# Kernel tuning notes

Measured on AMD Instinct MI355X. Metric: run time of the kernel, lower is better.

## Reference

```python
import jax, jax.numpy as jnp
import numpy as np

B, T, V, H = 256, 2048, 128, 64  # batch, seq_len, vocab/input_size, hidden_size


def setup_inputs() -> dict:
    key = jax.random.key(0)
    ks = jax.random.split(key, 11)
    s = 0.1  # weight scale
    d = jnp.float32
    return {
        "x": jax.random.normal(ks[0], (B, T, V), dtype=d),
        "W_f": jax.random.normal(ks[1], (V + H, H), dtype=d) * s,
        "b_f": jax.random.normal(ks[2], (H,), dtype=d) * s,
        "W_if": jax.random.normal(ks[3], (V + H, H), dtype=d) * s,
        "b_if": jax.random.normal(ks[4], (H,), dtype=d) * s,
        "W_ic": jax.random.normal(ks[5], (V + H, H), dtype=d) * s,
        "b_ic": jax.random.normal(ks[6], (H,), dtype=d) * s,
        "W_o": jax.random.normal(ks[7], (V + H, H), dtype=d) * s,
        "b_o": jax.random.normal(ks[8], (H,), dtype=d) * s,
        "W_out": jax.random.normal(ks[9], (H, V), dtype=d) * s,
        "b_out": jax.random.normal(ks[10], (V,), dtype=d) * s,
    }


def reference(x, W_f, b_f, W_if, b_if, W_ic, b_ic, W_o, b_o, W_out, b_out):
    # Manual LSTM cell from the source, stepped over time with lax.scan.
    # Per step (faithful to forward()+getOut()):
    #   s = concat(x_t, h);  f = sigmoid(s@W_f+b_f);  c = c*f
    #   add = tanh(s@W_ic+b_ic); af = sigmoid(s@W_if+b_if); c = c + add*af
    #   o = sigmoid(s@W_o+b_o);  h = tanh(c)*o
    #   out = softmax(h@W_out+b_out)
    b, t = x.shape[0], x.shape[1]
    h0 = jnp.zeros((b, W_f.shape[1]), dtype=x.dtype)
    c0 = jnp.zeros_like(h0)

    def step(carry, x_t):
        h, c = carry
        s = jnp.concatenate([x_t, h], axis=1)          # [B, V+H]
        f = jax.nn.sigmoid(s @ W_f + b_f)
        add = jnp.tanh(s @ W_ic + b_ic)
        af = jax.nn.sigmoid(s @ W_if + b_if)
        c = c * f + add * af
        o = jax.nn.sigmoid(s @ W_o + b_o)
        h = jnp.tanh(c) * o
        out = jax.nn.softmax(h @ W_out + b_out, axis=-1)  # [B, V]
        return (h, c), out

    (_, _), outs = jax.lax.scan(step, (h0, c0), jnp.swapaxes(x, 0, 1))
    return jnp.swapaxes(outs, 0, 1)  # [B, T, V]
```

## Files before the change

kernel.cpp:

```cpp
#include <hip/hip_runtime.h>
#include <cstdint>
#include <cstddef>

#define BB 256
#define TT 2048
#define VV 128
#define HH 64

typedef __attribute__((ext_vector_type(8))) short short8;
typedef __attribute__((ext_vector_type(4))) float f32x4;
typedef __attribute__((ext_vector_type(2))) float f32x2;

__device__ __forceinline__ float frcp(float x){ return __builtin_amdgcn_rcpf(x); }
__device__ __forceinline__ float sigm(float x){ return frcp(1.f + __expf(-x)); }
__device__ __forceinline__ float tanh_f(float x){ return 1.f - 2.f*frcp(1.f + __expf(2.f*x)); }

__device__ __forceinline__ void bar_lds(){
  asm volatile("s_waitcnt lgkmcnt(0)" ::: "memory");
  __builtin_amdgcn_s_barrier();
  __builtin_amdgcn_sched_barrier(0);
}

__device__ __forceinline__ void gload16(const void* g, void* l){
  __builtin_amdgcn_global_load_lds(
      (const __attribute__((address_space(1))) void*)g,
      (__attribute__((address_space(3))) void*)l, 16, 0, 0);
}

__device__ __forceinline__ unsigned short bf16hi(float x){
  unsigned u = __float_as_uint(x);
  return (unsigned short)((u + 0x7fffu + ((u>>16)&1u)) >> 16);
}
__device__ __forceinline__ void splitpack(const float* v8, short8& hi, short8& lo){
  #pragma unroll
  for (int j=0;j<8;++j){
    unsigned short h = bf16hi(v8[j]);
    float fh = __uint_as_float(((unsigned)h)<<16);
    unsigned short lw = bf16hi(v8[j] - fh);
    hi[j] = (short)h; lo[j] = (short)lw;
  }
}

__device__ __forceinline__ float qsum(float v){
  int t1 = __builtin_amdgcn_update_dpp(0, __float_as_int(v), 0xB1, 0xF, 0xF, true);
  v += __int_as_float(t1);
  int t2 = __builtin_amdgcn_update_dpp(0, __float_as_int(v), 0x4E, 0xF, 0xF, true);
  v += __int_as_float(t2);
  return v;
}

template<int CTRL>
__device__ __forceinline__ float dppmov(float v){
  return __int_as_float(__builtin_amdgcn_update_dpp(0, __float_as_int(v), CTRL, 0xF, 0xF, true));
}

__device__ __forceinline__ void pkfma(f32x2& acc, f32x2 a, f32x2 b){
  asm volatile("v_pk_fma_f32 %0, %1, %2, %0" : "+v"(acc) : "v"(a), "v"(b));
}

__global__ __launch_bounds__(256) void conv_w_k(
  const float* __restrict__ Wf, const float* __restrict__ Wi,
  const float* __restrict__ Wc, const float* __restrict__ Wo,
  const float* __restrict__ Wout,
  unsigned short* __restrict__ W4h, unsigned short* __restrict__ W4l,
  unsigned short* __restrict__ WOh, unsigned short* __restrict__ WOl)
{
  const int idx = blockIdx.x*256 + threadIdx.x;
  if (idx < 32768){
    const int j = idx&7, l=(idx>>3)&63, kk=(idx>>9)&3, nt=idx>>11;
    const int k = kk*32 + (l>>4)*8 + j;
    const int n = nt*16 + (l&15);
    const int g = n&3, colw = n>>2;
    const float* Ws = (g==0)?Wf:((g==1)?Wi:((g==2)?Wc:Wo));
    const float v = Ws[k*HH + colw];
    const unsigned short h = bf16hi(v);
    const float fh = __uint_as_float(((unsigned)h)<<16);
    W4h[idx] = h; W4l[idx] = bf16hi(v - fh);
  }
  if (idx < 8192){
    const int j = idx&7, l=(idx>>3)&63, kk=(idx>>9)&1, jt=idx>>10;
    const int k = kk*32 + (l>>4)*8 + j;
    const int jc = jt*16 + (l&15);
    const float v = Wout[k*VV + jc];
    const unsigned short h = bf16hi(v);
    const float fh = __uint_as_float(((unsigned)h)<<16);
    WOh[idx] = h; WOl[idx] = bf16hi(v - fh);
  }
}

__global__ __launch_bounds__(512,1) void pre_gemm_k(
  const float* __restrict__ x, const unsigned short* __restrict__ W4h,
  const unsigned short* __restrict__ W4l, float* __restrict__ PRE)
{
  __shared__ __align__(16) unsigned short XFh[16384];
  __shared__ __align__(16) unsigned short XFl[16384];
  const int tid = threadIdx.x, wv = tid>>6, l = tid&63, b = blockIdx.x;

  short8 Bh[2][4], Bl[2][4];
  #pragma unroll
  for (int ntl=0; ntl<2; ++ntl){
    const int nt = wv*2 + ntl;
    #pragma unroll
    for (int kk=0; kk<4; ++kk){
      Bh[ntl][kk] = *(const short8*)(W4h + ((nt*4+kk)*64 + l)*8);
      Bl[ntl][kk] = *(const short8*)(W4l + ((nt*4+kk)*64 + l)*8);
    }
  }

  #pragma unroll 1
  for (int mt=0; mt<16; ++mt){
    const size_t base_row = (size_t)b*TT + mt*128;
    #pragma unroll
    for (int i=0;i<4;++i){
      const int G = tid*4+i;
      const int lf = G&63, kk=(G>>6)&3, m8=G>>8;
      const float* src = x + (base_row + m8*16 + (lf&15))*VV + kk*32 + (lf>>4)*8;
      const f32x4 u = *(const f32x4*)src;
      const f32x4 v = *(const f32x4*)(src+4);
      float tmp[8] = {u[0],u[1],u[2],u[3], v[0],v[1],v[2],v[3]};
      short8 hi, lo; splitpack(tmp, hi, lo);
      *(short8*)&XFh[(size_t)G*8] = hi;
      *(short8*)&XFl[(size_t)G*8] = lo;
    }
    bar_lds();
    for (int m8=0; m8<8; ++m8){
      short8 Ah[4], Al[4];
      #pragma unroll
      for (int kk=0;kk<4;++kk){
        Ah[kk] = *(const short8*)&XFh[((m8*4+kk)*64 + l)*8];
        Al[kk] = *(const short8*)&XFl[((m8*4+kk)*64 + l)*8];
      }
      #pragma unroll
      for (int ntl=0; ntl<2; ++ntl){
        f32x4 acc = {0.f,0.f,0.f,0.f};
        #pragma unroll
        for (int kk=0;kk<4;++kk){
          acc = __builtin_amdgcn_mfma_f32_16x16x32_bf16(Al[kk], Bh[ntl][kk], acc, 0,0,0);
          acc = __builtin_amdgcn_mfma_f32_16x16x32_bf16(Ah[kk], Bl[ntl][kk], acc, 0,0,0);
          acc = __builtin_amdgcn_mfma_f32_16x16x32_bf16(Ah[kk], Bh[ntl][kk], acc, 0,0,0);
        }
        const int nt = wv*2 + ntl;
        float* dst = PRE + (base_row + m8*16 + (l>>4)*4)*256 + nt*16 + (l&15);
        #pragma unroll
        for (int r=0;r<4;++r) dst[(size_t)r*256] = acc[r];
      }
    }
    bar_lds();
  }
}

__global__ __launch_bounds__(256,1) void recur8_k(
  const float* __restrict__ W_f, const float* __restrict__ b_f,
  const float* __restrict__ W_if, const float* __restrict__ b_if,
  const float* __restrict__ W_ic, const float* __restrict__ b_ic,
  const float* __restrict__ W_o,  const float* __restrict__ b_o,
  const float* __restrict__ PRE,  float* __restrict__ H)
{
  __shared__ __align__(16) float hring[32*HH];
  const int tid=threadIdx.x, wv=tid>>6, l=tid&63, b=blockIdx.x;
  const int col = wv*16 + (l>>2), q = l&3;
  const bool qb0 = (l&1)!=0, qb1 = (l&2)!=0;

  f32x2 wf2[8], wi2[8], wc2[8], wo2[8];
  #pragma unroll
  for (int m=0;m<8;++m){
    const size_t k0 = (size_t)(VV + q*16 + 2*m)*HH + col;
    wf2[m] = f32x2{W_f [k0], W_f [k0+HH]};
    wi2[m] = f32x2{W_if[k0], W_if[k0+HH]};
    wc2[m] = f32x2{W_ic[k0], W_ic[k0+HH]};
    wo2[m] = f32x2{W_o [k0], W_o [k0+HH]};
  }
  const float bq  = ((q==0)?b_f:(q==1)?b_if:(q==2)?b_ic:b_o)[col];
  const float sgn = (q==2)? 2.f : -1.f;
  const float aA  = (q==2)? -2.f : 1.f;
  const float aB  = (q==2)? 1.f : 0.f;

  const float* PREl = PRE + (size_t)b*TT*256 + wv*64 + l;
  float* Hb = H + (size_t)b*TT*HH;
  const f32x4* hring4 = (const f32x4*)hring;

  if (tid < HH) hring[31*HH + tid] = 0.f;

  float pf[8];
  #pragma unroll
  for (int j=0;j<8;++j) pf[j] = PREl[(size_t)j*256];

  bar_lds();

  float c_ = 0.f;
  int hoff = 31*16 + q*4;
  int woff = col;

  #pragma unroll 1
  for (int t8=0; t8<TT; t8+=8){
    #pragma unroll
    for (int j=0;j<8;++j){
      const int t = t8+j;
      if (wv==1 && t>0 && (t&15)==0){
        #pragma unroll
        for (int i=0;i<4;++i){
          const int rt = t-16 + i*4 + (l>>4);
          const f32x4 v = hring4[(rt&31)*16 + (l&15)];
          *(f32x4*)(Hb + (size_t)rt*HH + (l&15)*4) = v;
        }
      }
      const f32x4 h0 = hring4[hoff+0], h1 = hring4[hoff+1];
      const f32x4 h2 = hring4[hoff+2], h3 = hring4[hoff+3];
      const float nxt = PREl[(size_t)((t+8)&(TT-1))*256];
      const float pq = pf[j];
      f32x2 a0={0.f,0.f}, a1={0.f,0.f}, a2={0.f,0.f}, a3={0.f,0.f};
      {
        const f32x2 p0 = f32x2{h0[0],h0[1]}, p1 = f32x2{h0[2],h0[3]};
        const f32x2 p2 = f32x2{h1[0],h1[1]}, p3 = f32x2{h1[2],h1[3]};
        const f32x2 p4 = f32x2{h2[0],h2[1]}, p5 = f32x2{h2[2],h2[3]};
        const f32x2 p6 = f32x2{h3[0],h3[1]}, p7 = f32x2{h3[2],h3[3]};
        pkfma(a0,p0,wf2[0]); pkfma(a0,p1,wf2[1]); pkfma(a0,p2,wf2[2]); pkfma(a0,p3,wf2[3]);
        pkfma(a0,p4,wf2[4]); pkfma(a0,p5,wf2[5]); pkfma(a0,p6,wf2[6]); pkfma(a0,p7,wf2[7]);
        pkfma(a1,p0,wi2[0]); pkfma(a1,p1,wi2[1]); pkfma(a1,p2,wi2[2]); pkfma(a1,p3,wi2[3]);
        pkfma(a1,p4,wi2[4]); pkfma(a1,p5,wi2[5]); pkfma(a1,p6,wi2[6]); pkfma(a1,p7,wi2[7]);
        pkfma(a2,p0,wc2[0]); pkfma(a2,p1,wc2[1]); pkfma(a2,p2,wc2[2]); pkfma(a2,p3,wc2[3]);
        pkfma(a2,p4,wc2[4]); pkfma(a2,p5,wc2[5]); pkfma(a2,p6,wc2[6]); pkfma(a2,p7,wc2[7]);
        pkfma(a3,p0,wo2[0]); pkfma(a3,p1,wo2[1]); pkfma(a3,p2,wo2[2]); pkfma(a3,p3,wo2[3]);
        pkfma(a3,p4,wo2[4]); pkfma(a3,p5,wo2[5]); pkfma(a3,p6,wo2[6]); pkfma(a3,p7,wo2[7]);
      }
      const float a0s = a0[0]+a0[1];
      const float a1s = a1[0]+a1[1];
      const float a2s = a2[0]+a2[1];
      const float a3s = a3[0]+a3[1];
      float tA = qb0 ? a1s : a0s;
      float tB = qb0 ? a0s : a1s;
      tA += dppmov<0xB1>(tB);
      float tC = qb0 ? a3s : a2s;
      float tD = qb0 ? a2s : a3s;
      tC += dppmov<0xB1>(tD);
      float r  = qb1 ? tC : tA;
      float rr = qb1 ? tA : tC;
      r += dppmov<0x4E>(rr);
      const float xx  = r + pq + bq;
      const float e   = __expf(sgn*xx);
      const float rc  = frcp(1.f + e);
      const float act = fmaf(aA, rc, aB);
      const float f_  = dppmov<0x00>(act);
      const float af  = dppmov<0x55>(act);
      const float ad  = dppmov<0xAA>(act);
      const float o_  = dppmov<0xFF>(act);
      c_ = c_*f_ + ad*af;
      const float hv = tanh_f(c_) * o_;
      if (q==0) hring[woff] = hv;
      pf[j] = nxt;
      hoff = (hoff + 16) & 511;
      woff = (woff + 64) & 2047;
      bar_lds();
    }
  }
  if (wv==1){
    #pragma unroll
    for (int i=0;i<4;++i){
      const int rt = TT-16 + i*4 + (l>>4);
      const f32x4 v = hring4[(rt&31)*16 + (l&15)];
      *(f32x4*)(Hb + (size_t)rt*HH + (l&15)*4) = v;
    }
  }
}

__global__ __launch_bounds__(512,1) void logit_k(
  const float* __restrict__ H, const unsigned short* __restrict__ WOh,
  const unsigned short* __restrict__ WOl, const float* __restrict__ b_out,
  float* __restrict__ out)
{
  const int tid=threadIdx.x, wv=tid>>6, l=tid&63, b=blockIdx.x;
  short8 Bh[8][2], Bl[8][2];
  #pragma unroll
  for (int jt=0;jt<8;++jt){
    #pragma unroll
    for (int kk=0;kk<2;++kk){
      Bh[jt][kk] = *(const short8*)(WOh + ((jt*2+kk)*64 + l)*8);
      Bl[jt][kk] = *(const short8*)(WOl + ((jt*2+kk)*64 + l)*8);
    }
  }
  float bj[8];
  #pragma unroll
  for (int jt=0;jt<8;++jt) bj[jt] = b_out[jt*16 + (l&15)];

  #pragma unroll 1
  for (int mt=0; mt<16; ++mt){
    const size_t row0 = (size_t)b*TT + mt*128 + wv*16;
    const float* hbase = H + (row0 + (l&15))*HH;
    short8 Ah[2], Al[2];
    #pragma unroll
    for (int kk=0;kk<2;++kk){
      const float* s = hbase + kk*32 + (l>>4)*8;
      const f32x4 u = *(const f32x4*)s;
      const f32x4 v = *(const f32x4*)(s+4);
      float tmp[8] = {u[0],u[1],u[2],u[3], v[0],v[1],v[2],v[3]};
      splitpack(tmp, Ah[kk], Al[kk]);
    }
    f32x4 acc[8];
    #pragma unroll
    for (int jt=0;jt<8;++jt){
      f32x4 a = {0.f,0.f,0.f,0.f};
      #pragma unroll
      for (int kk=0;kk<2;++kk){
        a = __builtin_amdgcn_mfma_f32_16x16x32_bf16(Al[kk], Bh[jt][kk], a, 0,0,0);
        a = __builtin_amdgcn_mfma_f32_16x16x32_bf16(Ah[kk], Bl[jt][kk], a, 0,0,0);
        a = __builtin_amdgcn_mfma_f32_16x16x32_bf16(Ah[kk], Bh[jt][kk], a, 0,0,0);
      }
      acc[jt] = a;
    }
    #pragma unroll
    for (int r=0;r<4;++r){
      float z[8];
      #pragma unroll
      for (int jt=0;jt<8;++jt) z[jt] = acc[jt][r] + bj[jt];
      float mx = z[0];
      #pragma unroll
      for (int jt=1;jt<8;++jt) mx = fmaxf(mx, z[jt]);
      mx = fmaxf(mx, __shfl_xor(mx,1));
      mx = fmaxf(mx, __shfl_xor(mx,2));
      mx = fmaxf(mx, __shfl_xor(mx,4));
      mx = fmaxf(mx, __shfl_xor(mx,8));
      float sum = 0.f;
      #pragma unroll
      for (int jt=0;jt<8;++jt){ z[jt] = __expf(z[jt]-mx); sum += z[jt]; }
      sum += __shfl_xor(sum,1);
      sum += __shfl_xor(sum,2);
      sum += __shfl_xor(sum,4);
      sum += __shfl_xor(sum,8);
      const float rs = frcp(sum);
      float* op = out + (row0 + (l>>4)*4 + r)*VV + (l&15);
      #pragma unroll
      for (int jt=0;jt<8;++jt) op[jt*16] = z[jt]*rs;
    }
  }
}

#define XA_IDX(buf,kk,q,s) ((buf)*2048 + (((kk)*4+(q))*16+(s))*8)
#define HA_IDX(buf,kk,q,s) ((buf)*1024 + (((kk)*4+(q))*16+(s))*8)
#define NBF 128

__device__ __forceinline__ void gload16f(const float* g, float* l){
  __builtin_amdgcn_global_load_lds(
      (const __attribute__((address_space(1))) void*)g,
      (__attribute__((address_space(3))) void*)l, 16, 0, 0);
}

__global__ __launch_bounds__(512, 1) void fused_fb_k(
  const float* __restrict__ x,
  const float* __restrict__ W_f,  const float* __restrict__ b_f,
  const float* __restrict__ W_if, const float* __restrict__ b_if,
  const float* __restrict__ W_ic, const float* __restrict__ b_ic,
  const float* __restrict__ W_o,  const float* __restrict__ b_o,
  const float* __restrict__ W_out,const float* __restrict__ b_out,
  float* __restrict__ out)
{
  __shared__ __align__(16) float XR[4*16*VV];
  __shared__ __align__(16) short XAh[2*2048];
  __shared__ __align__(16) short XAl[2*2048];
  __shared__ __align__(16) float PRE[32*256];
  __shared__ __align__(16) short HAh[2*1024];
  __shared__ __align__(16) short HAl[2*1024];
  __shared__ __align__(16) float HR[32*HH];

  const int tid = threadIdx.x;
  const int wv  = tid >> 6;
  const int l   = tid & 63;
  const int row = blockIdx.x;
  const float* xrow = x   + (size_t)row*TT*VV;
  float*       orow = out + (size_t)row*TT*VV;

  if (wv < 4) {
    const int col = (wv&3)*16 + (l>>2);
    const int q   = l&3;
    float wh0[16], wh1[16], wh2[16], wh3[16];
    #pragma unroll
    for (int m=0;m<16;++m){
      const size_t kidx = (size_t)(VV + q*16 + m)*HH + col;
      wh0[m]=W_f[kidx]; wh1[m]=W_if[kidx]; wh2[m]=W_ic[kidx]; wh3[m]=W_o[kidx];
    }
    const float b0=b_f[col], b1=b_if[col], b2=b_ic[col], b3=b_o[col];
    if (tid < HH) HR[31*HH + tid] = 0.f;
    bar_lds(); bar_lds(); bar_lds();
    float c = 0.f;
    #pragma unroll 1
    for (int t=0; t<TT; ++t){
      const f32x4* hp = (const f32x4*)&HR[((t+31)&31)*HH + q*16];
      const f32x4 pre4 = *(const f32x4*)&PRE[(t&31)*256 + col*4];
      float d0=0.f,d1=0.f,d2=0.f,d3=0.f;
      #pragma unroll
      for (int m=0;m<4;++m){
        const f32x4 hv = hp[m];
        #pragma unroll
        for (int e=0;e<4;++e){
          const float s = hv[e];
          d0 = fmaf(s, wh0[m*4+e], d0);
          d1 = fmaf(s, wh1[m*4+e], d1);
          d2 = fmaf(s, wh2[m*4+e], d2);
          d3 = fmaf(s, wh3[m*4+e], d3);
        }
      }
      d0 = qsum(d0); d1 = qsum(d1); d2 = qsum(d2); d3 = qsum(d3);
      const float f  = sigm(d0 + pre4[0] + b0);
      const float fi = sigm(d1 + pre4[1] + b1);
      const float ci = tanh_f(d2 + pre4[2] + b2);
      const float o  = sigm(d3 + pre4[3] + b3);
      c = c*f + ci*fi;
      const float hv2 = tanh_f(c) * o;
      if (q==0) HR[(t&31)*HH + col] = hv2;
      bar_lds();
    }
    bar_lds();
  } else {
    const int pv = wv - 4;
    const int pt = pv*64 + l;
    short8 Bh[4][4], Bl[4][4];
    #pragma unroll
    for (int ntl=0; ntl<4; ++ntl){
      const int n = (pv*4+ntl)*16 + (l&15);
      const int g = n&3, colw = n>>2;
      const float* Ws = (g==0)?W_f:((g==1)?W_if:((g==2)?W_ic:W_o));
      #pragma unroll
      for (int kk=0;kk<4;++kk){
        float tmp[8];
        #pragma unroll
        for (int j=0;j<8;++j) tmp[j] = Ws[(size_t)(kk*32+(l>>4)*8+j)*HH + colw];
        splitpack(tmp, Bh[ntl][kk], Bl[ntl][kk]);
      }
    }
    short8 Lh[2][2], Ll[2][2];
    #pragma unroll
    for (int jt=0; jt<2; ++jt){
      const int j = (pv*2+jt)*16 + (l&15);
      #pragma unroll
      for (int kk=0;kk<2;++kk){
        float tmp[8];
        #pragma unroll
        for (int jj=0;jj<8;++jj) tmp[jj] = W_out[(size_t)(kk*32+(l>>4)*8+jj)*VV + j];
        splitpack(tmp, Lh[jt][kk], Ll[jt][kk]);
      }
    }
    auto GLOAD = [&](int bb){
      #pragma unroll
      for (int i=0;i<2;++i){
        const float* src = xrow + (size_t)bb*16*VV + pv*512 + i*256 + l*4;
        float* dst = &XR[(bb&3)*2048 + pv*512 + i*256];
        gload16f(src, dst);
      }
    };
    auto CONV = [&](int bb){
      if (pt < 256){
        const int buf=bb&1, kk=pt>>6, qq=(pt>>4)&3, s=pt&15;
        const float* src = &XR[(bb&3)*2048 + s*VV + kk*32 + qq*8];
        float tmp[8];
        #pragma unroll
        for (int j=0;j<8;++j) tmp[j] = src[j];
        short8 hi, lo; splitpack(tmp, hi, lo);
        *(short8*)&XAh[XA_IDX(buf,kk,qq,s)] = hi;
        *(short8*)&XAl[XA_IDX(buf,kk,qq,s)] = lo;
      }
    };
    auto PREB = [&](int bb){
      const int buf = bb&1;
      short8 Ah[4], Al[4];
      #pragma unroll
      for (int kk=0;kk<4;++kk){
        Ah[kk] = *(const short8*)&XAh[XA_IDX(buf,kk,(l>>4),(l&15))];
        Al[kk] = *(const short8*)&XAl[XA_IDX(buf,kk,(l>>4),(l&15))];
      }
      #pragma unroll
      for (int ntl=0; ntl<4; ++ntl){
        f32x4 acc = {0.f,0.f,0.f,0.f};
        #pragma unroll
        for (int kk=0;kk<4;++kk){
          acc = __builtin_amdgcn_mfma_f32_16x16x32_bf16(Al[kk], Bh[ntl][kk], acc, 0,0,0);
          acc = __builtin_amdgcn_mfma_f32_16x16x32_bf16(Ah[kk], Bl[ntl][kk], acc, 0,0,0);
          acc = __builtin_amdgcn_mfma_f32_16x16x32_bf16(Ah[kk], Bh[ntl][kk], acc, 0,0,0);
        }
        const int n  = (pv*4+ntl)*16 + (l&15);
        const int s0 = buf*16 + (l>>4)*4;
        #pragma unroll
        for (int r=0;r<4;++r) PRE[(s0+r)*256 + n] = acc[r];
      }
    };
    auto LOGB = [&](int bb){
      const int buf = bb&1;
      short8 Ah[2], Al[2];
      #pragma unroll
      for (int kk=0;kk<2;++kk){
        Ah[kk] = *(const short8*)&HAh[HA_IDX(buf,kk,(l>>4),(l&15))];
        Al[kk] = *(const short8*)&HAl[HA_IDX(buf,kk,(l>>4),(l&15))];
      }
      #pragma unroll
      for (int jt=0; jt<2; ++jt){
        f32x4 acc = {0.f,0.f,0.f,0.f};
        #pragma unroll
        for (int kk=0;kk<2;++kk){
          acc = __builtin_amdgcn_mfma_f32_16x16x32_bf16(Al[kk], Lh[jt][kk], acc, 0,0,0);
          acc = __builtin_amdgcn_mfma_f32_16x16x32_bf16(Ah[kk], Ll[jt][kk], acc, 0,0,0);
          acc = __builtin_amdgcn_mfma_f32_16x16x32_bf16(Ah[kk], Lh[jt][kk], acc, 0,0,0);
        }
        const int j  = (pv*2+jt)*16 + (l&15);
        const int t0 = bb*16 + (l>>4)*4;
        #pragma unroll
        for (int r=0;r<4;++r) orow[(size_t)(t0+r)*VV + j] = acc[r];
      }
    };
    auto RELAY = [&](int hs2){
      if (pt < 8){
        const int kk = pt>>2, qq = pt&3;
        const int buf = (hs2>>4)&1, s = hs2&15;
        const float* src = &HR[(hs2&31)*HH + kk*32 + qq*8];
        float tmp[8];
        #pragma unroll
        for (int j=0;j<8;++j) tmp[j] = src[j];
        short8 hi, lo; splitpack(tmp, hi, lo);
        *(short8*)&HAh[HA_IDX(buf,kk,qq,s)] = hi;
        *(short8*)&HAl[HA_IDX(buf,kk,qq,s)] = lo;
      }
    };
    GLOAD(0); GLOAD(1); GLOAD(2);
    asm volatile("s_waitcnt vmcnt(2)" ::: "memory");
    bar_lds();
    CONV(0); CONV(1);
    bar_lds();
    PREB(0);
    bar_lds();
    #pragma unroll 1
    for (int t=0; t<TT; ++t){
      if (t >= 1) RELAY(t-1);
      const int slot = t&15, blk = t>>4;
      if (slot==0){ if (blk+1 < NBF) PREB(blk+1); }
      else if (slot==1){ if (blk >= 1) LOGB(blk-1); }
      else if (slot==2){ if (blk+3 < NBF) GLOAD(blk+3); }
      else if (slot==3){ if (blk+2 < NBF) asm volatile("s_waitcnt vmcnt(2)" ::: "memory"); }
      else if (slot==4){ if (blk+2 < NBF) CONV(blk+2); }
      bar_lds();
    }
    RELAY(TT-1);
    bar_lds();
    LOGB(NBF-1);
  }
}

__global__ __launch_bounds__(256) void softmax_fb_k(float* __restrict__ out)
{
  const int r = blockIdx.x*4 + (threadIdx.x>>6);
  const int l = threadIdx.x & 63;
  float2* p = (float2*)(out + (size_t)r*VV);
  float2 v = p[l];
  float m = fmaxf(v.x, v.y);
  #pragma unroll
  for (int d=1; d<64; d<<=1) m = fmaxf(m, __shfl_xor(m, d));
  float e0 = __expf(v.x - m), e1 = __expf(v.y - m);
  float s = e0 + e1;
  #pragma unroll
  for (int d=1; d<64; d<<=1) s += __shfl_xor(s, d);
  float rs = frcp(s);
  p[l] = make_float2(e0*rs, e1*rs);
}

extern "C" void kernel_launch(void* const* d_in, const int* in_sizes, int n_in,
                              void* d_out, int out_size, void* d_ws, size_t ws_size,
                              hipStream_t stream) {
  const float* x     = (const float*)d_in[0];
  const float* W_f   = (const float*)d_in[1];
  const float* b_f   = (const float*)d_in[2];
  const float* W_if  = (const float*)d_in[3];
  const float* b_if  = (const float*)d_in[4];
  const float* W_ic  = (const float*)d_in[5];
  const float* b_ic  = (const float*)d_in[6];
  const float* W_o   = (const float*)d_in[7];
  const float* b_o   = (const float*)d_in[8];
  const float* W_out = (const float*)d_in[9];
  const float* b_out = (const float*)d_in[10];
  float* out = (float*)d_out;

  const size_t PRE_B = (size_t)BB*TT*256*sizeof(float);
  const size_t H_B   = (size_t)BB*TT*HH*sizeof(float);
  const size_t need  = PRE_B + H_B + 2*32768*2 + 2*8192*2;

  if (ws_size >= need) {
    char* w = (char*)d_ws;
    float* PRE  = (float*)w;
    float* Hbuf = (float*)(w + PRE_B);
    unsigned short* W4h = (unsigned short*)(w + PRE_B + H_B);
    unsigned short* W4l = W4h + 32768;
    unsigned short* WOh = W4l + 32768;
    unsigned short* WOl = WOh + 8192;
    hipLaunchKernelGGL(conv_w_k, dim3(128), dim3(256), 0, stream,
                       W_f, W_if, W_ic, W_o, W_out, W4h, W4l, WOh, WOl);
    hipLaunchKernelGGL(pre_gemm_k, dim3(BB), dim3(512), 0, stream, x, W4h, W4l, PRE);
    hipLaunchKernelGGL(recur8_k, dim3(BB), dim3(256), 0, stream,
                       W_f, b_f, W_if, b_if, W_ic, b_ic, W_o, b_o, PRE, Hbuf);
    hipLaunchKernelGGL(logit_k, dim3(BB), dim3(512), 0, stream, Hbuf, WOh, WOl, b_out, out);
  } else {
    hipLaunchKernelGGL(fused_fb_k, dim3(BB), dim3(512), 0, stream,
                       x, W_f, b_f, W_if, b_if, W_ic, b_ic, W_o, b_o,
                       W_out, b_out, out);
    hipLaunchKernelGGL(softmax_fb_k, dim3(BB*TT/4), dim3(256), 0, stream, out);
  }
}
```

Before: 905.7 us.

## Interleave two batch rows per recurrence block to hide serial latency

The recurrence kernel now handles two independent batch rows per workgroup, launching half as many blocks. Each step computes both rows' gate dot products, DPP reductions and activations interleaved, sharing one barrier per step and the register-resident weights. This is meant to fill the latency bubbles of the serial dependency chain (LDS reads, DPP, exp/rcp, barrier) with independent work. In exchange each step has twice the ALU work, and only 128 blocks run, which leaves about half of the compute units idle.

Result: slower. 1.149 ms (+26.9%).

```diff
diff --git a/kernel.cpp b/kernel.cpp
--- a/kernel.cpp
+++ b/kernel.cpp
@@ -149,14 +149,14 @@
   }
 }
 
-__global__ __launch_bounds__(256,1) void recur8_k(
+__global__ __launch_bounds__(256,1) void recur9_k(
   const float* __restrict__ W_f, const float* __restrict__ b_f,
   const float* __restrict__ W_if, const float* __restrict__ b_if,
   const float* __restrict__ W_ic, const float* __restrict__ b_ic,
   const float* __restrict__ W_o,  const float* __restrict__ b_o,
   const float* __restrict__ PRE,  float* __restrict__ H)
 {
-  __shared__ __align__(16) float hring[32*HH];
+  __shared__ __align__(16) float hring[2*32*HH];
   const int tid=threadIdx.x, wv=tid>>6, l=tid&63, b=blockIdx.x;
   const int col = wv*16 + (l>>2), q = l&3;
   const bool qb0 = (l&1)!=0, qb1 = (l&2)!=0;
@@ -175,19 +175,22 @@
   const float aA  = (q==2)? -2.f : 1.f;
   const float aB  = (q==2)? 1.f : 0.f;
 
-  const float* PREl = PRE + (size_t)b*TT*256 + wv*64 + l;
-  float* Hb = H + (size_t)b*TT*HH;
+  const int rA = 2*b, rB = 2*b+1;
+  const float* PRElA = PRE + (size_t)rA*TT*256 + wv*64 + l;
+  const float* PRElB = PRE + (size_t)rB*TT*256 + wv*64 + l;
+  float* HbA = H + (size_t)rA*TT*HH;
+  float* HbB = H + (size_t)rB*TT*HH;
   const f32x4* hring4 = (const f32x4*)hring;
 
-  if (tid < HH) hring[31*HH + tid] = 0.f;
-
-  float pf[8];
-  #pragma unroll
-  for (int j=0;j<8;++j) pf[j] = PREl[(size_t)j*256];
+  if (tid < HH){ hring[31*HH + tid] = 0.f; hring[2048 + 31*HH + tid] = 0.f; }
+
+  float pfA[8], pfB[8];
+  #pragma unroll
+  for (int j=0;j<8;++j){ pfA[j] = PRElA[(size_t)j*256]; pfB[j] = PRElB[(size_t)j*256]; }
 
   bar_lds();
 
-  float c_ = 0.f;
+  float cA = 0.f, cB = 0.f;
   int hoff = 31*16 + q*4;
   int woff = col;
 
@@ -196,58 +199,71 @@
     #pragma unroll
     for (int j=0;j<8;++j){
       const int t = t8+j;
-      if (wv==1 && t>0 && (t&15)==0){
-        #pragma unroll
-        for (int i=0;i<4;++i){
-          const int rt = t-16 + i*4 + (l>>4);
-          const f32x4 v = hring4[(rt&31)*16 + (l&15)];
-          *(f32x4*)(Hb + (size_t)rt*HH + (l&15)*4) = v;
+      if (t>0 && (t&15)==0){
+        if (wv==1){
+          #pragma unroll
+          for (int i=0;i<4;++i){
+            const int rt = t-16 + i*4 + (l>>4);
+            const f32x4 v = hring4[(rt&31)*16 + (l&15)];
+            *(f32x4*)(HbA + (size_t)rt*HH + (l&15)*4) = v;
+          }
+        } else if (wv==2){
+          #pragma unroll
+          for (int i=0;i<4;++i){
+            const int rt = t-16 + i*4 + (l>>4);
+            const f32x4 v = hring4[512 + (rt&31)*16 + (l&15)];
+            *(f32x4*)(HbB + (size_t)rt*HH + (l&15)*4) = v;
+          }
         }
       }
-      const f32x4 h0 = hring4[hoff+0], h1 = hring4[hoff+1];
-      const f32x4 h2 = hring4[hoff+2], h3 = hring4[hoff+3];
-      const float nxt = PREl[(size_t)((t+8)&(TT-1))*256];
-      const float pq = pf[j];
-      f32x2 a0={0.f,0.f}, a1={0.f,0.f}, a2={0.f,0.f}, a3={0.f,0.f};
-      {
-        const f32x2 p0 = f32x2{h0[0],h0[1]}, p1 = f32x2{h0[2],h0[3]};
-        const f32x2 p2 = f32x2{h1[0],h1[1]}, p3 = f32x2{h1[2],h1[3]};
-        const f32x2 p4 = f32x2{h2[0],h2[1]}, p5 = f32x2{h2[2],h2[3]};
-        const f32x2 p6 = f32x2{h3[0],h3[1]}, p7 = f32x2{h3[2],h3[3]};
-        pkfma(a0,p0,wf2[0]); pkfma(a0,p1,wf2[1]); pkfma(a0,p2,wf2[2]); pkfma(a0,p3,wf2[3]);
-        pkfma(a0,p4,wf2[4]); pkfma(a0,p5,wf2[5]); pkfma(a0,p6,wf2[6]); pkfma(a0,p7,wf2[7]);
-        pkfma(a1,p0,wi2[0]); pkfma(a1,p1,wi2[1]); pkfma(a1,p2,wi2[2]); pkfma(a1,p3,wi2[3]);
-        pkfma(a1,p4,wi2[4]); pkfma(a1,p5,wi2[5]); pkfma(a1,p6,wi2[6]); pkfma(a1,p7,wi2[7]);
-        pkfma(a2,p0,wc2[0]); pkfma(a2,p1,wc2[1]); pkfma(a2,p2,wc2[2]); pkfma(a2,p3,wc2[3]);
-        pkfma(a2,p4,wc2[4]); pkfma(a2,p5,wc2[5]); pkfma(a2,p6,wc2[6]); pkfma(a2,p7,wc2[7]);
-        pkfma(a3,p0,wo2[0]); pkfma(a3,p1,wo2[1]); pkfma(a3,p2,wo2[2]); pkfma(a3,p3,wo2[3]);
-        pkfma(a3,p4,wo2[4]); pkfma(a3,p5,wo2[5]); pkfma(a3,p6,wo2[6]); pkfma(a3,p7,wo2[7]);
-      }
-      const float a0s = a0[0]+a0[1];
-      const float a1s = a1[0]+a1[1];
-      const float a2s = a2[0]+a2[1];
-      const float a3s = a3[0]+a3[1];
-      float tA = qb0 ? a1s : a0s;
-      float tB = qb0 ? a0s : a1s;
-      tA += dppmov<0xB1>(tB);
-      float tC = qb0 ? a3s : a2s;
-      float tD = qb0 ? a2s : a3s;
-      tC += dppmov<0xB1>(tD);
-      float r  = qb1 ? tC : tA;
-      float rr = qb1 ? tA : tC;
-      r += dppmov<0x4E>(rr);
-      const float xx  = r + pq + bq;
-      const float e   = __expf(sgn*xx);
-      const float rc  = frcp(1.f + e);
-      const float act = fmaf(aA, rc, aB);
-      const float f_  = dppmov<0x00>(act);
-      const float af  = dppmov<0x55>(act);
-      const float ad  = dppmov<0xAA>(act);
-      const float o_  = dppmov<0xFF>(act);
-      c_ = c_*f_ + ad*af;
-      const float hv = tanh_f(c_) * o_;
-      if (q==0) hring[woff] = hv;
-      pf[j] = nxt;
+      const f32x4 hA0 = hring4[hoff+0], hA1 = hring4[hoff+1];
+      const f32x4 hA2 = hring4[hoff+2], hA3 = hring4[hoff+3];
+      const f32x4 hB0 = hring4[512+hoff+0], hB1 = hring4[512+hoff+1];
+      const f32x4 hB2 = hring4[512+hoff+2], hB3 = hring4[512+hoff+3];
+      const float nxtA = PRElA[(size_t)((t+8)&(TT-1))*256];
+      const float nxtB = PRElB[(size_t)((t+8)&(TT-1))*256];
+      const float pqA = pfA[j], pqB = pfB[j];
+
+      const f32x2 pA[8] = { {hA0[0],hA0[1]},{hA0[2],hA0[3]},{hA1[0],hA1[1]},{hA1[2],hA1[3]},
+                            {hA2[0],hA2[1]},{hA2[2],hA2[3]},{hA3[0],hA3[1]},{hA3[2],hA3[3]} };
+      const f32x2 pB[8] = { {hB0[0],hB0[1]},{hB0[2],hB0[3]},{hB1[0],hB1[1]},{hB1[2],hB1[3]},
+                            {hB2[0],hB2[1]},{hB2[2],hB2[3]},{hB3[0],hB3[1]},{hB3[2],hB3[3]} };
+      f32x2 a0A={0,0},a1A={0,0},a2A={0,0},a3A={0,0};
+      f32x2 a0B={0,0},a1B={0,0},a2B={0,0},a3B={0,0};
+      #pragma unroll
+      for (int m=0;m<8;++m){
+        pkfma(a0A,pA[m],wf2[m]); pkfma(a1A,pA[m],wi2[m]);
+        pkfma(a2A,pA[m],wc2[m]); pkfma(a3A,pA[m],wo2[m]);
+        pkfma(a0B,pB[m],wf2[m]); pkfma(a1B,pB[m],wi2[m]);
+        pkfma(a2B,pB[m],wc2[m]); pkfma(a3B,pB[m],wo2[m]);
+      }
+      const float a0sA=a0A[0]+a0A[1], a1sA=a1A[0]+a1A[1], a2sA=a2A[0]+a2A[1], a3sA=a3A[0]+a3A[1];
+      const float a0sB=a0B[0]+a0B[1], a1sB=a1B[0]+a1B[1], a2sB=a2B[0]+a2B[1], a3sB=a3B[0]+a3B[1];
+      float tAA = qb0 ? a1sA : a0sA;  float tBA = qb0 ? a0sA : a1sA;
+      float tAB = qb0 ? a1sB : a0sB;  float tBB = qb0 ? a0sB : a1sB;
+      tAA += dppmov<0xB1>(tBA);       tAB += dppmov<0xB1>(tBB);
+      float tCA = qb0 ? a3sA : a2sA;  float tDA = qb0 ? a2sA : a3sA;
+      float tCB = qb0 ? a3sB : a2sB;  float tDB = qb0 ? a2sB : a3sB;
+      tCA += dppmov<0xB1>(tDA);       tCB += dppmov<0xB1>(tDB);
+      float rA_ = qb1 ? tCA : tAA;    float rrA = qb1 ? tAA : tCA;
+      float rB_ = qb1 ? tCB : tAB;    float rrB = qb1 ? tAB : tCB;
+      rA_ += dppmov<0x4E>(rrA);       rB_ += dppmov<0x4E>(rrB);
+      const float xxA = rA_ + pqA + bq;
+      const float xxB = rB_ + pqB + bq;
+      const float eA = __expf(sgn*xxA);
+      const float eB = __expf(sgn*xxB);
+      const float actA = fmaf(aA, frcp(1.f+eA), aB);
+      const float actB = fmaf(aA, frcp(1.f+eB), aB);
+      const float fA_ = dppmov<0x00>(actA), afA = dppmov<0x55>(actA);
+      const float adA = dppmov<0xAA>(actA), oA_ = dppmov<0xFF>(actA);
+      const float fB_ = dppmov<0x00>(actB), afB = dppmov<0x55>(actB);
+      const float adB = dppmov<0xAA>(actB), oB_ = dppmov<0xFF>(actB);
+      cA = cA*fA_ + adA*afA;
+      cB = cB*fB_ + adB*afB;
+      const float hvA = tanh_f(cA) * oA_;
+      const float hvB = tanh_f(cB) * oB_;
+      if (q==0){ hring[woff] = hvA; hring[2048+woff] = hvB; }
+      pfA[j] = nxtA; pfB[j] = nxtB;
       hoff = (hoff + 16) & 511;
       woff = (woff + 64) & 2047;
       bar_lds();
@@ -258,7 +274,14 @@
     for (int i=0;i<4;++i){
       const int rt = TT-16 + i*4 + (l>>4);
       const f32x4 v = hring4[(rt&31)*16 + (l&15)];
-      *(f32x4*)(Hb + (size_t)rt*HH + (l&15)*4) = v;
+      *(f32x4*)(HbA + (size_t)rt*HH + (l&15)*4) = v;
+    }
+  } else if (wv==2){
+    #pragma unroll
+    for (int i=0;i<4;++i){
+      const int rt = TT-16 + i*4 + (l>>4);
+      const f32x4 v = hring4[512 + (rt&31)*16 + (l&15)];
+      *(f32x4*)(HbB + (size_t)rt*HH + (l&15)*4) = v;
     }
   }
 }
@@ -589,7 +612,7 @@
     hipLaunchKernelGGL(conv_w_k, dim3(128), dim3(256), 0, stream,
                        W_f, W_if, W_ic, W_o, W_out, W4h, W4l, WOh, WOl);
     hipLaunchKernelGGL(pre_gemm_k, dim3(BB), dim3(512), 0, stream, x, W4h, W4l, PRE);
-    hipLaunchKernelGGL(recur8_k, dim3(BB), dim3(256), 0, stream,
+    hipLaunchKernelGGL(recur9_k, dim3(BB/2), dim3(256), 0, stream,
                        W_f, b_f, W_if, b_if, W_ic, b_ic, W_o, b_o, PRE, Hbuf);
     hipLaunchKernelGGL(logit_k, dim3(BB), dim3(512), 0, stream, Hbuf, WOh, WOl, b_out, out);
   } else {
```
